# Kernel optimization log

Measured on AMD Instinct MI355X. Metric: run time of the kernel, lower is better.

The kernel has to match this reference:

```python
import jax, jax.numpy as jnp
import numpy as np

S, D, H, HD = 3072, 1280, 16, 80
FF = 4 * D
EPS = 1e-6


def layernorm(x, scale, bias):
    mu = jnp.mean(x, axis=-1, keepdims=True)
    var = jnp.mean(jnp.square(x - mu), axis=-1, keepdims=True)
    return (x - mu) * jax.lax.rsqrt(var + EPS) * scale + bias


def rotate_half(x):
    x1 = x[..., : x.shape[-1] // 2]
    x2 = x[..., x.shape[-1] // 2 :]
    return jnp.concatenate([-x2, x1], axis=-1)


def apply_rope(x, freqs):
    # x: (S,H,hd), freqs: (S,hd/2)
    cos = jnp.repeat(jnp.cos(freqs), 2, axis=-1)[:, None, :]  # (S,1,hd)
    sin = jnp.repeat(jnp.sin(freqs), 2, axis=-1)[:, None, :]
    return x * cos + rotate_half(x) * sin


def quick_gelu(x):
    return x * jax.nn.sigmoid(1.702 * x)


def setup_inputs() -> dict:
    key = jax.random.key(0)
    ks = jax.random.split(key, 12)
    s = 0.02
    return {
        "hidden_states": jax.random.normal(ks[0], (S, D), jnp.float32),
        "rotary_pos_emb": jax.random.normal(ks[1], (S, HD // 2), jnp.float32),
        "ln1_scale": jnp.ones((D,), jnp.float32),
        "ln1_bias": jnp.zeros((D,), jnp.float32),
        "ln2_scale": jnp.ones((D,), jnp.float32),
        "ln2_bias": jnp.zeros((D,), jnp.float32),
        "qkv_w": jax.random.normal(ks[2], (D, 3 * D), jnp.float32) * s,
        "qkv_b": jnp.zeros((3 * D,), jnp.float32),
        "proj_w": jax.random.normal(ks[3], (D, D), jnp.float32) * s,
        "proj_b": jnp.zeros((D,), jnp.float32),
        "fc1_w": jax.random.normal(ks[4], (D, FF), jnp.float32) * s,
        "fc1_b": jnp.zeros((FF,), jnp.float32),
        "fc2_w": jax.random.normal(ks[5], (FF, D), jnp.float32) * s,
        "fc2_b": jnp.zeros((D,), jnp.float32),
        "cu_seqlens": jnp.array([0, 1024, 2048, 3072], jnp.int32),
    }


def reference(hidden_states, rotary_pos_emb, ln1_scale, ln1_bias, ln2_scale,
              ln2_bias, qkv_w, qkv_b, proj_w, proj_b, fc1_w, fc1_b, fc2_w,
              fc2_b, cu_seqlens):
    x = hidden_states  # (S, D)
    h = layernorm(x, ln1_scale, ln1_bias)
    qkv = (h @ qkv_w + qkv_b).reshape(S, 3, H, HD)
    q, k, v = qkv[:, 0], qkv[:, 1], qkv[:, 2]  # each (S, H, hd)
    q = apply_rope(q, rotary_pos_emb)
    k = apply_rope(k, rotary_pos_emb)

    # block-diagonal varlen mask from cu_seqlens (same segment attends)
    ids = jnp.arange(S)
    seg = jnp.searchsorted(cu_seqlens, ids, side="right")  # (S,)
    valid = seg[:, None] == seg[None, :]  # (S, S)
    bias = jnp.where(valid, 0.0, jnp.finfo(q.dtype).min)

    scale = 1.0 / jnp.sqrt(jnp.asarray(HD, q.dtype))
    scores = jnp.einsum("qhd,khd->hqk", q, k) * scale + bias
    probs = jax.nn.softmax(scores.astype(jnp.float32), axis=-1).astype(q.dtype)
    attn = jnp.einsum("hqk,khd->qhd", probs, v).reshape(S, D)
    attn = attn @ proj_w + proj_b

    x = x + attn
    h2 = layernorm(x, ln2_scale, ln2_bias)
    mlp = quick_gelu(h2 @ fc1_w + fc1_b) @ fc2_w + fc2_b
    return x + mlp
```

## Files before the change

### kernel.cpp

```cpp
#include <hip/hip_runtime.h>

typedef __bf16 bf16x8 __attribute__((ext_vector_type(8)));
typedef float f32x4 __attribute__((ext_vector_type(4)));
typedef unsigned short u16;
typedef u16 u16x4 __attribute__((ext_vector_type(4)));
typedef u16 u16x8 __attribute__((ext_vector_type(8)));
typedef float float4v __attribute__((ext_vector_type(4)));

__device__ __forceinline__ u16 f2bf(float f) {
    __bf16 b = (__bf16)f;
    return __builtin_bit_cast(unsigned short, b);
}
__device__ __forceinline__ float bf2f(u16 x) {
    __bf16 b = __builtin_bit_cast(__bf16, x);
    return (float)b;
}

__device__ __forceinline__ void gld16(const void* g, void* l) {
    __builtin_amdgcn_global_load_lds((const __attribute__((address_space(1))) void*)g,
                                     (__attribute__((address_space(3))) void*)l, 16, 0, 0);
}

__device__ __forceinline__ int xcd_swz(int orig, int nwg) {
    const int q = nwg >> 3, r = nwg & 7;
    const int xcd = orig & 7, pos = orig >> 3;
    return (xcd < r ? xcd * (q + 1) : r * (q + 1) + (xcd - r) * q) + pos;
}

__global__ __launch_bounds__(256) void transpose_all_kernel(
    const float* __restrict__ qkvw, const float* __restrict__ projw,
    const float* __restrict__ fc1w, const float* __restrict__ fc2w,
    u16* __restrict__ qkvwT, u16* __restrict__ projwT,
    u16* __restrict__ fc1wT, u16* __restrict__ fc2wT)
{
    __shared__ u16 tile[64][65];
    int bid = blockIdx.x;
    const float* W; u16* WT; int K, N, nx;
    if (bid < 1200)      { W = qkvw;  WT = qkvwT;  K = 1280; N = 3840; nx = 60; }
    else if (bid < 1600) { bid -= 1200; W = projw; WT = projwT; K = 1280; N = 1280; nx = 20; }
    else if (bid < 3200) { bid -= 1600; W = fc1w;  WT = fc1wT;  K = 1280; N = 5120; nx = 80; }
    else                 { bid -= 3200; W = fc2w;  WT = fc2wT;  K = 5120; N = 1280; nx = 20; }
    const int tx = threadIdx.x & 63, ty = threadIdx.x >> 6;
    const int n0 = (bid % nx) * 64, k0 = (bid / nx) * 64;
    #pragma unroll
    for (int i = ty; i < 64; i += 4)
        tile[i][tx] = f2bf(W[(size_t)(k0 + i) * N + n0 + tx]);
    __syncthreads();
    #pragma unroll
    for (int i = ty; i < 64; i += 4)
        WT[(size_t)(n0 + i) * K + k0 + tx] = tile[tx][i];
}

__global__ __launch_bounds__(256) void ln_kernel(
    const float* __restrict__ x, const float* __restrict__ sc,
    const float* __restrict__ bias, u16* __restrict__ out)
{
    const int row = blockIdx.x, t = threadIdx.x;
    const float* xr = x + (size_t)row * 1280;
    float v[5], s1 = 0.f, s2 = 0.f;
    #pragma unroll
    for (int i = 0; i < 5; i++) {
        v[i] = xr[t + i * 256];
        s1 += v[i];
        s2 += v[i] * v[i];
    }
    #pragma unroll
    for (int off = 32; off; off >>= 1) {
        s1 += __shfl_down(s1, off);
        s2 += __shfl_down(s2, off);
    }
    __shared__ float rA[4], rB[4];
    if ((t & 63) == 0) { rA[t >> 6] = s1; rB[t >> 6] = s2; }
    __syncthreads();
    s1 = rA[0] + rA[1] + rA[2] + rA[3];
    s2 = rB[0] + rB[1] + rB[2] + rB[3];
    const float mu = s1 * (1.f / 1280.f);
    const float var = s2 * (1.f / 1280.f) - mu * mu;
    const float rstd = rsqrtf(var + 1e-6f);
    #pragma unroll
    for (int i = 0; i < 5; i++) {
        const int d = t + i * 256;
        out[(size_t)row * 1280 + d] = f2bf((v[i] - mu) * rstd * sc[d] + bias[d]);
    }
}

__global__ __launch_bounds__(256) void reduce4_ln_kernel(
    const float* __restrict__ parts, const float* __restrict__ bias,
    const float* __restrict__ res, const float* __restrict__ lns,
    const float* __restrict__ lnb, float* __restrict__ xmid,
    u16* __restrict__ h2, size_t MN)
{
    const int row = blockIdx.x, t = threadIdx.x;
    float v[5], s1 = 0.f, s2 = 0.f;
    #pragma unroll
    for (int i = 0; i < 5; i++) {
        const int d = t + i * 256;
        const size_t idx = (size_t)row * 1280 + d;
        float a = parts[idx] + parts[MN + idx] + parts[2 * MN + idx] + parts[3 * MN + idx]
                + res[idx] + bias[d];
        v[i] = a;
        xmid[idx] = a;
        s1 += a;
        s2 += a * a;
    }
    #pragma unroll
    for (int off = 32; off; off >>= 1) {
        s1 += __shfl_down(s1, off);
        s2 += __shfl_down(s2, off);
    }
    __shared__ float rA[4], rB[4];
    if ((t & 63) == 0) { rA[t >> 6] = s1; rB[t >> 6] = s2; }
    __syncthreads();
    s1 = rA[0] + rA[1] + rA[2] + rA[3];
    s2 = rB[0] + rB[1] + rB[2] + rB[3];
    const float mu = s1 * (1.f / 1280.f);
    const float var = s2 * (1.f / 1280.f) - mu * mu;
    const float rstd = rsqrtf(var + 1e-6f);
    #pragma unroll
    for (int i = 0; i < 5; i++) {
        const int d = t + i * 256;
        h2[(size_t)row * 1280 + d] = f2bf((v[i] - mu) * rstd * lns[d] + lnb[d]);
    }
}

template <int GELU, int OUTB, int SPLIT>
__global__ __launch_bounds__(512, 2) void gemm256_kernel(
    const u16* __restrict__ A, const u16* __restrict__ BT,
    const float* __restrict__ bias,
    float* __restrict__ outF, u16* __restrict__ outB,
    int M, int N, int K)
{
    __shared__ u16 As[2][256 * 64];
    __shared__ u16 Bs[2][256 * 64];
    const int tid = threadIdx.x, lane = tid & 63, wave = tid >> 6;
    const int nwg = gridDim.x * gridDim.y;
    const int bid = xcd_swz(blockIdx.y * gridDim.x + blockIdx.x, nwg);
    const int m0 = (bid / gridDim.x) * 256, n0 = (bid % gridDim.x) * 256;
    const int wr = wave >> 2, wc = wave & 3;
    const int wm = wr * 128, wn = wc * 64;
    const int lr = lane & 15, lh = lane >> 4;

    const int kchunk = K / SPLIT;
    const int kz = (SPLIT > 1) ? blockIdx.z : 0;
    const int kbeg = kz * kchunk;
    const int niter = kchunk >> 7;

    const int sr = lane >> 3;
    const int sc8 = (lane & 7) ^ sr;

    f32x4 acc[8][4] = {};
    bf16x8 bq[4][2];

    auto stgA = [&](int t, int h) {
        const int buf = t & 1;
        #pragma unroll
        for (int j = 0; j < 2; j++) {
            const int row = h * 128 + j * 64 + wave * 8 + sr;
            gld16(A + (size_t)(m0 + row) * K + kbeg + t * 64 + sc8 * 8,
                  &As[buf][h * 8192 + j * 4096 + wave * 512]);
        }
    };
    auto stgB = [&](int t, int h) {
        const int buf = t & 1;
        #pragma unroll
        for (int j = 0; j < 2; j++) {
            const int row = h * 128 + j * 64 + wave * 8 + sr;
            gld16(BT + (size_t)(n0 + row) * K + kbeg + t * 64 + sc8 * 8,
                  &Bs[buf][h * 8192 + j * 4096 + wave * 512]);
        }
    };

#define PHASE(BUF, Q, STGSTMT, WAITSTMT)                                        \
    {                                                                           \
        if ((Q) == 0) {                                                         \
            _Pragma("unroll") for (int ni = 0; ni < 4; ni++) {                  \
                const int row = wn + ni * 16 + lr;                              \
                _Pragma("unroll") for (int kk = 0; kk < 2; kk++)                \
                    bq[ni][kk] = *reinterpret_cast<const bf16x8*>(              \
                        &Bs[BUF][row * 64 + ((kk * 4 + lh) ^ (row & 7)) * 8]);  \
            }                                                                   \
        }                                                                       \
        bf16x8 afq[2][2];                                                       \
        _Pragma("unroll") for (int m2 = 0; m2 < 2; m2++) {                      \
            const int row = wm + (Q) * 32 + m2 * 16 + lr;                       \
            _Pragma("unroll") for (int kk = 0; kk < 2; kk++)                    \
                afq[m2][kk] = *reinterpret_cast<const bf16x8*>(                 \
                    &As[BUF][row * 64 + ((kk * 4 + lh) ^ (row & 7)) * 8]);      \
        }                                                                       \
        STGSTMT;                                                                \
        __builtin_amdgcn_s_barrier();                                           \
        asm volatile("s_waitcnt lgkmcnt(0)" ::: "memory");                      \
        __builtin_amdgcn_s_setprio(1);                                          \
        _Pragma("unroll") for (int kk = 0; kk < 2; kk++)                        \
            _Pragma("unroll") for (int m2 = 0; m2 < 2; m2++)                    \
                _Pragma("unroll") for (int ni = 0; ni < 4; ni++)                \
                    acc[(Q) * 2 + m2][ni] =                                     \
                        __builtin_amdgcn_mfma_f32_16x16x32_bf16(                \
                            afq[m2][kk], bq[ni][kk], acc[(Q) * 2 + m2][ni],     \
                            0, 0, 0);                                           \
        __builtin_amdgcn_s_setprio(0);                                          \
        WAITSTMT;                                                               \
        __builtin_amdgcn_s_barrier();                                           \
    }

    stgB(0, 0); stgB(0, 1);
    stgA(0, 0); stgA(0, 1);
    stgB(1, 0); stgB(1, 1);
    asm volatile("s_waitcnt vmcnt(4)" ::: "memory");
    __builtin_amdgcn_s_barrier();

    for (int i = 0; i < niter - 1; i++) {
        const int t0 = 2 * i, t1 = 2 * i + 1;
        PHASE(0, 0, stgA(t1, 0), (void)0);
        PHASE(0, 1, stgA(t1, 1), (void)0);
        PHASE(0, 2, stgB(t0 + 2, 0), (void)0);
        PHASE(0, 3, stgB(t0 + 2, 1),
              asm volatile("s_waitcnt vmcnt(4)" ::: "memory"));
        PHASE(1, 0, stgA(t0 + 2, 0), (void)0);
        PHASE(1, 1, stgA(t0 + 2, 1), (void)0);
        PHASE(1, 2, stgB(t1 + 2, 0), (void)0);
        PHASE(1, 3, stgB(t1 + 2, 1),
              asm volatile("s_waitcnt vmcnt(4)" ::: "memory"));
    }
    {
        const int t1 = 2 * niter - 1;
        PHASE(0, 0, stgA(t1, 0), (void)0);
        PHASE(0, 1, stgA(t1, 1), (void)0);
        PHASE(0, 2, (void)0, (void)0);
        PHASE(0, 3, (void)0,
              asm volatile("s_waitcnt vmcnt(0)" ::: "memory"));
        PHASE(1, 0, (void)0, (void)0);
        PHASE(1, 1, (void)0, (void)0);
        PHASE(1, 2, (void)0, (void)0);
        PHASE(1, 3, (void)0, (void)0);
    }
#undef PHASE

    if (SPLIT > 1) {
        float* pf = outF + (size_t)kz * M * N;
        #pragma unroll
        for (int mi = 0; mi < 8; mi++)
            #pragma unroll
            for (int ni = 0; ni < 4; ni++) {
                const int col = n0 + wn + ni * 16 + lr;
                #pragma unroll
                for (int r = 0; r < 4; r++) {
                    const int rowg = m0 + wm + mi * 16 + lh * 4 + r;
                    pf[(size_t)rowg * N + col] = acc[mi][ni][r];
                }
            }
        return;
    }

    #pragma unroll
    for (int mi = 0; mi < 8; mi++) {
        #pragma unroll
        for (int ni = 0; ni < 4; ni++) {
            const int col = n0 + wn + ni * 16 + lr;
            const float bv = bias[col];
            #pragma unroll
            for (int r = 0; r < 4; r++) {
                const int rowg = m0 + wm + mi * 16 + lh * 4 + r;
                float v = acc[mi][ni][r] + bv;
                if (GELU) v = v * (1.0f / (1.0f + __expf(-1.702f * v)));
                if (OUTB) outB[(size_t)rowg * N + col] = f2bf(v);
            }
        }
    }
}

template <int GELU, int RES, int OUTF, int OUTB, int SPLIT>
__global__ __launch_bounds__(256) void gemm_kernel(
    const u16* __restrict__ A, const u16* __restrict__ BT,
    const float* __restrict__ bias, const float* __restrict__ res,
    float* __restrict__ outF, u16* __restrict__ outB,
    int M, int N, int K)
{
    __shared__ u16 As[128 * 64];
    __shared__ u16 Bs[128 * 64];
    const int tid = threadIdx.x, lane = tid & 63, wave = tid >> 6;
    const int nwg = gridDim.x * gridDim.y;
    const int bid = xcd_swz(blockIdx.y * gridDim.x + blockIdx.x, nwg);
    const int m0 = (bid / gridDim.x) * 128, n0 = (bid % gridDim.x) * 128;
    const int wm = (wave >> 1) * 64, wn = (wave & 1) * 64;
    const int lr = lane & 15, lh = lane >> 4;
    const int srow = lane >> 3;
    const int schunk = (lane & 7) ^ (srow & 7);

    const int kchunk = K / SPLIT;
    const int kz = (SPLIT > 1) ? blockIdx.z : 0;
    const int kbeg = kz * kchunk, kend = kbeg + kchunk;

    f32x4 acc[4][4] = {};

    for (int k0 = kbeg; k0 < kend; k0 += 64) {
        #pragma unroll
        for (int s = 0; s < 4; s++) {
            const int seg = wave + s * 4;
            const int row = seg * 8 + srow;
            gld16(A + (size_t)(m0 + row) * K + k0 + schunk * 8, &As[seg * 512]);
            gld16(BT + (size_t)(n0 + row) * K + k0 + schunk * 8, &Bs[seg * 512]);
        }
        asm volatile("s_waitcnt vmcnt(0)" ::: "memory");
        __syncthreads();

        bf16x8 af[4][2], bfr[4][2];
        #pragma unroll
        for (int mi = 0; mi < 4; mi++) {
            const int row = wm + mi * 16 + lr;
            #pragma unroll
            for (int kk = 0; kk < 2; kk++) {
                const int cb = (kk * 64 + lh * 16) ^ ((row & 7) << 4);
                af[mi][kk] = *reinterpret_cast<const bf16x8*>((const char*)As + row * 128 + cb);
            }
        }
        #pragma unroll
        for (int ni = 0; ni < 4; ni++) {
            const int row = wn + ni * 16 + lr;
            #pragma unroll
            for (int kk = 0; kk < 2; kk++) {
                const int cb = (kk * 64 + lh * 16) ^ ((row & 7) << 4);
                bfr[ni][kk] = *reinterpret_cast<const bf16x8*>((const char*)Bs + row * 128 + cb);
            }
        }
        #pragma unroll
        for (int kk = 0; kk < 2; kk++)
            #pragma unroll
            for (int mi = 0; mi < 4; mi++)
                #pragma unroll
                for (int ni = 0; ni < 4; ni++)
                    acc[mi][ni] = __builtin_amdgcn_mfma_f32_16x16x32_bf16(
                        af[mi][kk], bfr[ni][kk], acc[mi][ni], 0, 0, 0);
        __syncthreads();
    }

    if (SPLIT > 1) {
        float* pf = outF + (size_t)kz * M * N;
        #pragma unroll
        for (int mi = 0; mi < 4; mi++)
            #pragma unroll
            for (int ni = 0; ni < 4; ni++) {
                const int col = n0 + wn + ni * 16 + lr;
                #pragma unroll
                for (int r = 0; r < 4; r++) {
                    const int rowg = m0 + wm + mi * 16 + lh * 4 + r;
                    pf[(size_t)rowg * N + col] = acc[mi][ni][r];
                }
            }
        return;
    }

    #pragma unroll
    for (int mi = 0; mi < 4; mi++) {
        #pragma unroll
        for (int ni = 0; ni < 4; ni++) {
            const int col = n0 + wn + ni * 16 + lr;
            const float bv = bias[col];
            #pragma unroll
            for (int r = 0; r < 4; r++) {
                const int rowg = m0 + wm + mi * 16 + lh * 4 + r;
                float v = acc[mi][ni][r] + bv;
                if (RES) v += res[(size_t)rowg * N + col];
                if (GELU) v = v * (1.0f / (1.0f + __expf(-1.702f * v)));
                if (OUTF) outF[(size_t)rowg * N + col] = v;
                if (OUTB) outB[(size_t)rowg * N + col] = f2bf(v);
            }
        }
    }
}

__global__ __launch_bounds__(256) void reduce4_kernel(
    const float* __restrict__ parts, const float* __restrict__ bias,
    const float* __restrict__ res, float* __restrict__ out, int N, size_t MN)
{
    const size_t i4 = ((size_t)blockIdx.x * 256 + threadIdx.x) * 4;
    if (i4 >= MN) return;
    float4v a = *reinterpret_cast<const float4v*>(parts + i4);
    a += *reinterpret_cast<const float4v*>(parts + MN + i4);
    a += *reinterpret_cast<const float4v*>(parts + 2 * MN + i4);
    a += *reinterpret_cast<const float4v*>(parts + 3 * MN + i4);
    a += *reinterpret_cast<const float4v*>(res + i4);
    const int col = (int)(i4 % N);
    a += *reinterpret_cast<const float4v*>(bias + col);
    *reinterpret_cast<float4v*>(out + i4) = a;
}

__global__ __launch_bounds__(256) void rope_kernel(
    const u16* __restrict__ qkv, const float* __restrict__ freqs,
    u16* __restrict__ qp, u16* __restrict__ kp, u16* __restrict__ vt)
{
    const int s = blockIdx.x, t = threadIdx.x;
    const float scale = 0.1118033988749895f;
    __shared__ float cs[40], sn[40];
    if (t < 40) {
        const float f = freqs[(size_t)s * 40 + t];
        cs[t] = cosf(f);
        sn[t] = sinf(f);
    }
    __syncthreads();
    const u16* row = qkv + (size_t)s * 3840;
    for (int i = t; i < 1280; i += 256) {
        const int h = i / 80, d = i % 80;
        const float c = cs[d >> 1], sv = sn[d >> 1];
        const float q0 = bf2f(row[i]);
        const float q1 = (d < 40) ? -bf2f(row[i + 40]) : bf2f(row[i - 40]);
        qp[((size_t)h * 3072 + s) * 96 + d] = f2bf((q0 * c + q1 * sv) * scale);
        const float k0 = bf2f(row[1280 + i]);
        const float k1 = (d < 40) ? -bf2f(row[1280 + i + 40]) : bf2f(row[1280 + i - 40]);
        kp[((size_t)h * 3072 + s) * 128 + d] = f2bf(k0 * c + k1 * sv);
        vt[((size_t)h * 80 + d) * 3072 + s] = row[2560 + i];
    }
    {
        const int h = t / 16, d = 80 + (t % 16);
        qp[((size_t)h * 3072 + s) * 96 + d] = 0;
    }
    for (int i = t; i < 768; i += 256) {
        const int h = i / 48, d = 80 + (i % 48);
        kp[((size_t)h * 3072 + s) * 128 + d] = 0;
    }
}

__global__ __launch_bounds__(256) void attn_kernel(
    const u16* __restrict__ qp, const u16* __restrict__ kp,
    const u16* __restrict__ vt, u16* __restrict__ attn_out)
{
    const int tid = threadIdx.x, lane = tid & 63, wave = tid >> 6;
    const int w = xcd_swz(blockIdx.x, 768);
    const int qt = w & 15;
    const int h = (w >> 4) & 15;
    const int sq = w >> 8;
    const int lr = lane & 15, lh = lane >> 4;
    const int qrow = sq * 1024 + qt * 64 + wave * 16;

    __shared__ u16 Ks[2][64 * 128];
    __shared__ u16 Vs[2][80 * 64];

    bf16x8 aq[3];
    {
        const u16* qb = qp + ((size_t)h * 3072 + qrow + lr) * 96 + lh * 8;
        #pragma unroll
        for (int d0 = 0; d0 < 3; d0++)
            aq[d0] = *reinterpret_cast<const bf16x8*>(qb + d0 * 32);
    }

    float m = -1e30f, l = 0.f;
    f32x4 acc[5] = {};

    const u16* kseg = kp + ((size_t)h * 3072 + sq * 1024) * 128;
    const u16* vseg = vt + (size_t)h * 80 * 3072 + sq * 1024;

    const int krow_l = lane >> 4;
    const int kch    = lane & 15;
    const int vrow_l = lane >> 3;
    const int vch    = lane & 7;

    auto stageK = [&](int t, int buf) {
        #pragma unroll
        for (int s = 0; s < 4; s++) {
            const int seg = wave + s * 4;
            const int row = seg * 4 + krow_l;
            gld16(kseg + (size_t)(t * 64 + row) * 128 + ((kch ^ (row & 7)) * 8),
                  &Ks[buf][seg * 512]);
        }
    };
    auto stageV = [&](int t, int buf) {
        #pragma unroll
        for (int s = 0; s < 3; s++) {
            const int seg = wave + s * 4;
            if (seg < 10) {
                const int row = seg * 8 + vrow_l;
                gld16(vseg + (size_t)row * 3072 + t * 64 + ((vch ^ (row & 7)) * 8),
                      &Vs[buf][seg * 512]);
            }
        }
    };

    stageK(0, 0);
    stageV(0, 0);
    asm volatile("s_waitcnt vmcnt(0)" ::: "memory");
    __syncthreads();

    const int prow = wave * 16 + lr;
    const int psw = prow & 7;

    for (int t = 0; t < 16; t++) {
        const int cur = t & 1;
        if (t < 15) {
            stageK(t + 1, cur ^ 1);
            stageV(t + 1, cur ^ 1);
        }

        f32x4 sc[4] = {};
        #pragma unroll
        for (int c = 0; c < 4; c++) {
            #pragma unroll
            for (int d0 = 0; d0 < 3; d0++) {
                const int row = c * 16 + lr;
                const int rb = row * 256 + (((d0 * 4 + lh) ^ (row & 7)) << 4);
                bf16x8 kf = *reinterpret_cast<const bf16x8*>((const char*)Ks[cur] + rb);
                sc[c] = __builtin_amdgcn_mfma_f32_16x16x32_bf16(kf, aq[d0], sc[c], 0, 0, 0);
            }
        }

        float pmax = sc[0][0];
        #pragma unroll
        for (int c = 0; c < 4; c++)
            #pragma unroll
            for (int r = 0; r < 4; r++)
                pmax = fmaxf(pmax, sc[c][r]);
        pmax = fmaxf(pmax, __shfl_xor(pmax, 16));
        pmax = fmaxf(pmax, __shfl_xor(pmax, 32));

        if (!__all(pmax - m <= 8.0f)) {
            const float mn = fmaxf(m, pmax);
            const float fac = __expf(m - mn);
            m = mn;
            l *= fac;
            #pragma unroll
            for (int df = 0; df < 5; df++)
                #pragma unroll
                for (int r = 0; r < 4; r++)
                    acc[df][r] *= fac;
        }

        float p[4][4], rs = 0.f;
        #pragma unroll
        for (int c = 0; c < 4; c++)
            #pragma unroll
            for (int r = 0; r < 4; r++) {
                p[c][r] = __expf(sc[c][r] - m);
                rs += p[c][r];
            }
        rs += __shfl_xor(rs, 16);
        rs += __shfl_xor(rs, 32);
        l += rs;

        char* pb = (char*)Ks[cur] + prow * 256;
        const int prd = ((12 + lh) ^ psw) << 4;

        #pragma unroll
        for (int cc = 0; cc < 2; cc++) {
            u16x4 pw;
            #pragma unroll
            for (int r = 0; r < 4; r++)
                pw[r] = f2bf(p[cc][r]);
            *reinterpret_cast<u16x4*>(
                pb + (((12 + cc * 2 + (lh >> 1)) ^ psw) << 4) + (lh & 1) * 8) = pw;
        }
        asm volatile("s_waitcnt lgkmcnt(0)" ::: "memory");
        {
            bf16x8 pa = *reinterpret_cast<const bf16x8*>(pb + prd);
            asm volatile("s_waitcnt lgkmcnt(0)" ::: "memory");
            #pragma unroll
            for (int df = 0; df < 5; df++) {
                const int row = df * 16 + lr;
                const int vb = row * 128 + ((lh ^ (row & 7)) << 4);
                bf16x8 vf = *reinterpret_cast<const bf16x8*>((const char*)Vs[cur] + vb);
                acc[df] = __builtin_amdgcn_mfma_f32_16x16x32_bf16(vf, pa, acc[df], 0, 0, 0);
            }
        }
        #pragma unroll
        for (int cc = 0; cc < 2; cc++) {
            u16x4 pw;
            #pragma unroll
            for (int r = 0; r < 4; r++)
                pw[r] = f2bf(p[2 + cc][r]);
            *reinterpret_cast<u16x4*>(
                pb + (((12 + cc * 2 + (lh >> 1)) ^ psw) << 4) + (lh & 1) * 8) = pw;
        }
        asm volatile("s_waitcnt lgkmcnt(0)" ::: "memory");
        {
            bf16x8 pa = *reinterpret_cast<const bf16x8*>(pb + prd);
            #pragma unroll
            for (int df = 0; df < 5; df++) {
                const int row = df * 16 + lr;
                const int vb = row * 128 + (((4 + lh) ^ (row & 7)) << 4);
                bf16x8 vf = *reinterpret_cast<const bf16x8*>((const char*)Vs[cur] + vb);
                acc[df] = __builtin_amdgcn_mfma_f32_16x16x32_bf16(vf, pa, acc[df], 0, 0, 0);
            }
        }

        asm volatile("s_waitcnt vmcnt(0)" ::: "memory");
        __syncthreads();
    }

    const float invl = 1.0f / l;
    u16* orow = attn_out + (size_t)(qrow + lr) * 1280 + h * 80;
    #pragma unroll
    for (int df = 0; df < 5; df++) {
        u16x4 o;
        #pragma unroll
        for (int r = 0; r < 4; r++)
            o[r] = f2bf(acc[df][r] * invl);
        *reinterpret_cast<u16x4*>(orow + df * 16 + lh * 4) = o;
    }
}

extern "C" void kernel_launch(void* const* d_in, const int* in_sizes, int n_in,
                              void* d_out, int out_size, void* d_ws, size_t ws_size,
                              hipStream_t stream) {
    const float* hidden = (const float*)d_in[0];
    const float* rot    = (const float*)d_in[1];
    const float* ln1s   = (const float*)d_in[2];
    const float* ln1b   = (const float*)d_in[3];
    const float* ln2s   = (const float*)d_in[4];
    const float* ln2b   = (const float*)d_in[5];
    const float* qkvw   = (const float*)d_in[6];
    const float* qkvb   = (const float*)d_in[7];
    const float* projw  = (const float*)d_in[8];
    const float* projb  = (const float*)d_in[9];
    const float* fc1w   = (const float*)d_in[10];
    const float* fc1b   = (const float*)d_in[11];
    const float* fc2w   = (const float*)d_in[12];
    const float* fc2b   = (const float*)d_in[13];
    float* out = (float*)d_out;

    char* p = (char*)d_ws;
    auto alloc = [&](size_t n) { char* r = p; p += (n + 255) & ~(size_t)255; return r; };
    u16* qkvwT  = (u16*)alloc((size_t)3840 * 1280 * 2);
    u16* projwT = (u16*)alloc((size_t)1280 * 1280 * 2);
    u16* fc1wT  = (u16*)alloc((size_t)5120 * 1280 * 2);
    u16* fc2wT  = (u16*)alloc((size_t)1280 * 5120 * 2);
    u16* hbuf   = (u16*)alloc((size_t)3072 * 1280 * 2);
    u16* qkvbf  = (u16*)alloc((size_t)3072 * 5120 * 2);
    u16* attnb  = (u16*)alloc((size_t)3072 * 1280 * 2);
    float* xmid = (float*)alloc((size_t)3072 * 1280 * 4);
    float* parts = (float*)alloc((size_t)4 * 3072 * 1280 * 4);
    u16* qp2 = (u16*)parts;
    u16* kp2 = qp2 + (size_t)16 * 3072 * 96;
    u16* vt2 = kp2 + (size_t)16 * 3072 * 128;
    u16* h2   = hbuf;
    u16* mlp1 = qkvbf;
    const size_t MN = (size_t)3072 * 1280;

    transpose_all_kernel<<<4800, 256, 0, stream>>>(
        qkvw, projw, fc1w, fc2w, qkvwT, projwT, fc1wT, fc2wT);

    ln_kernel<<<3072, 256, 0, stream>>>(hidden, ln1s, ln1b, hbuf);
    gemm256_kernel<0, 1, 1><<<dim3(15, 12), 512, 0, stream>>>(
        hbuf, qkvwT, qkvb, nullptr, qkvbf, 3072, 3840, 1280);
    rope_kernel<<<3072, 256, 0, stream>>>(qkvbf, rot, qp2, kp2, vt2);
    attn_kernel<<<768, 256, 0, stream>>>(qp2, kp2, vt2, attnb);
    gemm_kernel<0, 0, 1, 0, 4><<<dim3(10, 24, 4), 256, 0, stream>>>(
        attnb, projwT, projb, nullptr, parts, nullptr, 3072, 1280, 1280);
    reduce4_ln_kernel<<<3072, 256, 0, stream>>>(
        parts, projb, hidden, ln2s, ln2b, xmid, h2, MN);
    gemm256_kernel<1, 1, 1><<<dim3(20, 12), 512, 0, stream>>>(
        h2, fc1wT, fc1b, nullptr, mlp1, 3072, 5120, 1280);
    gemm256_kernel<0, 0, 4><<<dim3(5, 12, 4), 512, 0, stream>>>(
        mlp1, fc2wT, fc2b, parts, nullptr, 3072, 1280, 5120);
    reduce4_kernel<<<(int)(MN / 4 / 256), 256, 0, stream>>>(parts, fc2b, xmid, out, 1280, MN);
}
```

Baseline: 289.5 us.

## Store split-K partials in bf16 and precompute LDS/global address pointers

Split-K partial sums from the projection and fc2 GEMMs are now written and read as bf16 instead of fp32. This halves the traffic for the partials buffer and for the reduce kernels that sum them. Separately, the GEMM and attention kernels precompute per-thread global and LDS address pointers outside their loops, which cuts the integer address arithmetic inside the inner loops. Rounding the partials to bf16 adds accuracy loss to the residual path.

```diff
diff --git a/kernel.cpp b/kernel.cpp
--- a/kernel.cpp
+++ b/kernel.cpp
@@ -85,7 +85,7 @@
 }
 
 __global__ __launch_bounds__(256) void reduce4_ln_kernel(
-    const float* __restrict__ parts, const float* __restrict__ bias,
+    const u16* __restrict__ parts, const float* __restrict__ bias,
     const float* __restrict__ res, const float* __restrict__ lns,
     const float* __restrict__ lnb, float* __restrict__ xmid,
     u16* __restrict__ h2, size_t MN)
@@ -96,7 +96,8 @@
     for (int i = 0; i < 5; i++) {
         const int d = t + i * 256;
         const size_t idx = (size_t)row * 1280 + d;
-        float a = parts[idx] + parts[MN + idx] + parts[2 * MN + idx] + parts[3 * MN + idx]
+        float a = bf2f(parts[idx]) + bf2f(parts[MN + idx])
+                + bf2f(parts[2 * MN + idx]) + bf2f(parts[3 * MN + idx])
                 + res[idx] + bias[d];
         v[i] = a;
         xmid[idx] = a;
@@ -121,6 +122,24 @@
         const int d = t + i * 256;
         h2[(size_t)row * 1280 + d] = f2bf((v[i] - mu) * rstd * lns[d] + lnb[d]);
     }
+}
+
+__global__ __launch_bounds__(256) void reduce4b_kernel(
+    const u16* __restrict__ parts, const float* __restrict__ bias,
+    const float* __restrict__ res, float* __restrict__ out, int N, size_t MN)
+{
+    const size_t i4 = ((size_t)blockIdx.x * 256 + threadIdx.x) * 4;
+    if (i4 >= MN) return;
+    float4v a = *reinterpret_cast<const float4v*>(res + i4);
+    #pragma unroll
+    for (int p = 0; p < 4; p++) {
+        u16x4 v = *reinterpret_cast<const u16x4*>(parts + p * MN + i4);
+        #pragma unroll
+        for (int r = 0; r < 4; r++) a[r] += bf2f(v[r]);
+    }
+    const int col = (int)(i4 % N);
+    a += *reinterpret_cast<const float4v*>(bias + col);
+    *reinterpret_cast<float4v*>(out + i4) = a;
 }
 
 template <int GELU, int OUTB, int SPLIT>
@@ -139,6 +158,7 @@
     const int wr = wave >> 2, wc = wave & 3;
     const int wm = wr * 128, wn = wc * 64;
     const int lr = lane & 15, lh = lane >> 4;
+    const int xa = lr & 7;
 
     const int kchunk = K / SPLIT;
     const int kz = (SPLIT > 1) ? blockIdx.z : 0;
@@ -151,42 +171,47 @@
     f32x4 acc[8][4] = {};
     bf16x8 bq[4][2];
 
-    auto stgA = [&](int t, int h) {
-        const int buf = t & 1;
+    const char* aRd[2] = {
+        (const char*)As + (wm + lr) * 128 + ((0 + lh) ^ xa) * 16,
+        (const char*)As + (wm + lr) * 128 + ((4 + lh) ^ xa) * 16 };
+    const char* bRd[2] = {
+        (const char*)Bs + (wn + lr) * 128 + ((0 + lh) ^ xa) * 16,
+        (const char*)Bs + (wn + lr) * 128 + ((4 + lh) ^ xa) * 16 };
+
+    const u16 *aG[2][2], *bG[2][2];
+    #pragma unroll
+    for (int h = 0; h < 2; h++)
         #pragma unroll
         for (int j = 0; j < 2; j++) {
             const int row = h * 128 + j * 64 + wave * 8 + sr;
-            gld16(A + (size_t)(m0 + row) * K + kbeg + t * 64 + sc8 * 8,
-                  &As[buf][h * 8192 + j * 4096 + wave * 512]);
-        }
+            aG[h][j] = A + (size_t)(m0 + row) * K + kbeg + sc8 * 8;
+            bG[h][j] = BT + (size_t)(n0 + row) * K + kbeg + sc8 * 8;
+        }
+
+    auto stgA = [&](int t, int h) {
+        u16* d = (u16*)As + (t & 1) * 16384 + h * 8192 + wave * 512;
+        gld16(aG[h][0] + (size_t)t * 64, d);
+        gld16(aG[h][1] + (size_t)t * 64, d + 4096);
     };
     auto stgB = [&](int t, int h) {
-        const int buf = t & 1;
-        #pragma unroll
-        for (int j = 0; j < 2; j++) {
-            const int row = h * 128 + j * 64 + wave * 8 + sr;
-            gld16(BT + (size_t)(n0 + row) * K + kbeg + t * 64 + sc8 * 8,
-                  &Bs[buf][h * 8192 + j * 4096 + wave * 512]);
-        }
+        u16* d = (u16*)Bs + (t & 1) * 16384 + h * 8192 + wave * 512;
+        gld16(bG[h][0] + (size_t)t * 64, d);
+        gld16(bG[h][1] + (size_t)t * 64, d + 4096);
     };
 
 #define PHASE(BUF, Q, STGSTMT, WAITSTMT)                                        \
     {                                                                           \
         if ((Q) == 0) {                                                         \
-            _Pragma("unroll") for (int ni = 0; ni < 4; ni++) {                  \
-                const int row = wn + ni * 16 + lr;                              \
+            _Pragma("unroll") for (int ni = 0; ni < 4; ni++)                    \
                 _Pragma("unroll") for (int kk = 0; kk < 2; kk++)                \
                     bq[ni][kk] = *reinterpret_cast<const bf16x8*>(              \
-                        &Bs[BUF][row * 64 + ((kk * 4 + lh) ^ (row & 7)) * 8]);  \
-            }                                                                   \
+                        bRd[kk] + (BUF) * 32768 + ni * 2048);                   \
         }                                                                       \
         bf16x8 afq[2][2];                                                       \
-        _Pragma("unroll") for (int m2 = 0; m2 < 2; m2++) {                      \
-            const int row = wm + (Q) * 32 + m2 * 16 + lr;                       \
+        _Pragma("unroll") for (int m2 = 0; m2 < 2; m2++)                        \
             _Pragma("unroll") for (int kk = 0; kk < 2; kk++)                    \
                 afq[m2][kk] = *reinterpret_cast<const bf16x8*>(                 \
-                    &As[BUF][row * 64 + ((kk * 4 + lh) ^ (row & 7)) * 8]);      \
-        }                                                                       \
+                    aRd[kk] + (BUF) * 32768 + (Q) * 4096 + m2 * 2048);          \
         STGSTMT;                                                                \
         __builtin_amdgcn_s_barrier();                                           \
         asm volatile("s_waitcnt lgkmcnt(0)" ::: "memory");                      \
@@ -237,7 +262,7 @@
 #undef PHASE
 
     if (SPLIT > 1) {
-        float* pf = outF + (size_t)kz * M * N;
+        u16* pf = outB + (size_t)kz * M * N;
         #pragma unroll
         for (int mi = 0; mi < 8; mi++)
             #pragma unroll
@@ -246,7 +271,7 @@
                 #pragma unroll
                 for (int r = 0; r < 4; r++) {
                     const int rowg = m0 + wm + mi * 16 + lh * 4 + r;
-                    pf[(size_t)rowg * N + col] = acc[mi][ni][r];
+                    pf[(size_t)rowg * N + col] = f2bf(acc[mi][ni][r]);
                 }
             }
         return;
@@ -269,12 +294,10 @@
     }
 }
 
-template <int GELU, int RES, int OUTF, int OUTB, int SPLIT>
+template <int SPLIT>
 __global__ __launch_bounds__(256) void gemm_kernel(
     const u16* __restrict__ A, const u16* __restrict__ BT,
-    const float* __restrict__ bias, const float* __restrict__ res,
-    float* __restrict__ outF, u16* __restrict__ outB,
-    int M, int N, int K)
+    u16* __restrict__ partB, int M, int N, int K)
 {
     __shared__ u16 As[128 * 64];
     __shared__ u16 Bs[128 * 64];
@@ -284,45 +307,54 @@
     const int m0 = (bid / gridDim.x) * 128, n0 = (bid % gridDim.x) * 128;
     const int wm = (wave >> 1) * 64, wn = (wave & 1) * 64;
     const int lr = lane & 15, lh = lane >> 4;
+    const int xa = lr & 7;
     const int srow = lane >> 3;
     const int schunk = (lane & 7) ^ (srow & 7);
 
     const int kchunk = K / SPLIT;
     const int kz = (SPLIT > 1) ? blockIdx.z : 0;
-    const int kbeg = kz * kchunk, kend = kbeg + kchunk;
+    const int kbeg = kz * kchunk;
+
+    const u16 *aG[4], *bG[4];
+    u16 *dA[4], *dB[4];
+    #pragma unroll
+    for (int s = 0; s < 4; s++) {
+        const int seg = wave + s * 4;
+        const int row = seg * 8 + srow;
+        aG[s] = A + (size_t)(m0 + row) * K + kbeg + schunk * 8;
+        bG[s] = BT + (size_t)(n0 + row) * K + kbeg + schunk * 8;
+        dA[s] = As + seg * 512;
+        dB[s] = Bs + seg * 512;
+    }
+    const char* aRd[2] = {
+        (const char*)As + (wm + lr) * 128 + ((0 + lh) ^ xa) * 16,
+        (const char*)As + (wm + lr) * 128 + ((4 + lh) ^ xa) * 16 };
+    const char* bRd[2] = {
+        (const char*)Bs + (wn + lr) * 128 + ((0 + lh) ^ xa) * 16,
+        (const char*)Bs + (wn + lr) * 128 + ((4 + lh) ^ xa) * 16 };
 
     f32x4 acc[4][4] = {};
 
-    for (int k0 = kbeg; k0 < kend; k0 += 64) {
+    for (int ko = 0; ko < kchunk; ko += 64) {
         #pragma unroll
         for (int s = 0; s < 4; s++) {
-            const int seg = wave + s * 4;
-            const int row = seg * 8 + srow;
-            gld16(A + (size_t)(m0 + row) * K + k0 + schunk * 8, &As[seg * 512]);
-            gld16(BT + (size_t)(n0 + row) * K + k0 + schunk * 8, &Bs[seg * 512]);
+            gld16(aG[s] + ko, dA[s]);
+            gld16(bG[s] + ko, dB[s]);
         }
         asm volatile("s_waitcnt vmcnt(0)" ::: "memory");
         __syncthreads();
 
         bf16x8 af[4][2], bfr[4][2];
         #pragma unroll
-        for (int mi = 0; mi < 4; mi++) {
-            const int row = wm + mi * 16 + lr;
-            #pragma unroll
-            for (int kk = 0; kk < 2; kk++) {
-                const int cb = (kk * 64 + lh * 16) ^ ((row & 7) << 4);
-                af[mi][kk] = *reinterpret_cast<const bf16x8*>((const char*)As + row * 128 + cb);
-            }
-        }
-        #pragma unroll
-        for (int ni = 0; ni < 4; ni++) {
-            const int row = wn + ni * 16 + lr;
-            #pragma unroll
-            for (int kk = 0; kk < 2; kk++) {
-                const int cb = (kk * 64 + lh * 16) ^ ((row & 7) << 4);
-                bfr[ni][kk] = *reinterpret_cast<const bf16x8*>((const char*)Bs + row * 128 + cb);
-            }
-        }
+        for (int mi = 0; mi < 4; mi++)
+            #pragma unroll
+            for (int kk = 0; kk < 2; kk++)
+                af[mi][kk] = *reinterpret_cast<const bf16x8*>(aRd[kk] + mi * 2048);
+        #pragma unroll
+        for (int ni = 0; ni < 4; ni++)
+            #pragma unroll
+            for (int kk = 0; kk < 2; kk++)
+                bfr[ni][kk] = *reinterpret_cast<const bf16x8*>(bRd[kk] + ni * 2048);
         #pragma unroll
         for (int kk = 0; kk < 2; kk++)
             #pragma unroll
@@ -334,55 +366,18 @@
         __syncthreads();
     }
 
-    if (SPLIT > 1) {
-        float* pf = outF + (size_t)kz * M * N;
-        #pragma unroll
-        for (int mi = 0; mi < 4; mi++)
-            #pragma unroll
-            for (int ni = 0; ni < 4; ni++) {
-                const int col = n0 + wn + ni * 16 + lr;
-                #pragma unroll
-                for (int r = 0; r < 4; r++) {
-                    const int rowg = m0 + wm + mi * 16 + lh * 4 + r;
-                    pf[(size_t)rowg * N + col] = acc[mi][ni][r];
-                }
-            }
-        return;
-    }
-
-    #pragma unroll
-    for (int mi = 0; mi < 4; mi++) {
+    u16* pf = partB + (size_t)kz * M * N;
+    #pragma unroll
+    for (int mi = 0; mi < 4; mi++)
         #pragma unroll
         for (int ni = 0; ni < 4; ni++) {
             const int col = n0 + wn + ni * 16 + lr;
-            const float bv = bias[col];
             #pragma unroll
             for (int r = 0; r < 4; r++) {
                 const int rowg = m0 + wm + mi * 16 + lh * 4 + r;
-                float v = acc[mi][ni][r] + bv;
-                if (RES) v += res[(size_t)rowg * N + col];
-                if (GELU) v = v * (1.0f / (1.0f + __expf(-1.702f * v)));
-                if (OUTF) outF[(size_t)rowg * N + col] = v;
-                if (OUTB) outB[(size_t)rowg * N + col] = f2bf(v);
+                pf[(size_t)rowg * N + col] = f2bf(acc[mi][ni][r]);
             }
         }
-    }
-}
-
-__global__ __launch_bounds__(256) void reduce4_kernel(
-    const float* __restrict__ parts, const float* __restrict__ bias,
-    const float* __restrict__ res, float* __restrict__ out, int N, size_t MN)
-{
-    const size_t i4 = ((size_t)blockIdx.x * 256 + threadIdx.x) * 4;
-    if (i4 >= MN) return;
-    float4v a = *reinterpret_cast<const float4v*>(parts + i4);
-    a += *reinterpret_cast<const float4v*>(parts + MN + i4);
-    a += *reinterpret_cast<const float4v*>(parts + 2 * MN + i4);
-    a += *reinterpret_cast<const float4v*>(parts + 3 * MN + i4);
-    a += *reinterpret_cast<const float4v*>(res + i4);
-    const int col = (int)(i4 % N);
-    a += *reinterpret_cast<const float4v*>(bias + col);
-    *reinterpret_cast<float4v*>(out + i4) = a;
 }
 
 __global__ __launch_bounds__(256) void rope_kernel(
@@ -430,6 +425,7 @@
     const int h = (w >> 4) & 15;
     const int sq = w >> 8;
     const int lr = lane & 15, lh = lane >> 4;
+    const int xa = lr & 7;
     const int qrow = sq * 1024 + qt * 64 + wave * 16;
 
     __shared__ u16 Ks[2][64 * 128];
@@ -454,25 +450,33 @@
     const int vrow_l = lane >> 3;
     const int vch    = lane & 7;
 
+    const u16 *kG[4], *vG[3];
+    u16 *kD[4], *vD[3];
+    #pragma unroll
+    for (int s = 0; s < 4; s++) {
+        const int seg = wave + s * 4;
+        const int row = seg * 4 + krow_l;
+        kG[s] = kseg + (size_t)row * 128 + ((kch ^ (row & 7)) * 8);
+        kD[s] = (u16*)Ks + seg * 512;
+    }
+    #pragma unroll
+    for (int s = 0; s < 3; s++) {
+        const int seg = wave + s * 4;
+        const int row = (seg < 10) ? seg * 8 + vrow_l : 0;
+        vG[s] = vseg + (size_t)row * 3072 + ((vch ^ (row & 7)) * 8);
+        vD[s] = (u16*)Vs + seg * 512;
+    }
+
     auto stageK = [&](int t, int buf) {
         #pragma unroll
-        for (int s = 0; s < 4; s++) {
-            const int seg = wave + s * 4;
-            const int row = seg * 4 + krow_l;
-            gld16(kseg + (size_t)(t * 64 + row) * 128 + ((kch ^ (row & 7)) * 8),
-                  &Ks[buf][seg * 512]);
-        }
+        for (int s = 0; s < 4; s++)
+            gld16(kG[s] + (size_t)t * 8192, kD[s] + buf * 8192);
     };
     auto stageV = [&](int t, int buf) {
         #pragma unroll
-        for (int s = 0; s < 3; s++) {
-            const int seg = wave + s * 4;
-            if (seg < 10) {
-                const int row = seg * 8 + vrow_l;
-                gld16(vseg + (size_t)row * 3072 + t * 64 + ((vch ^ (row & 7)) * 8),
-                      &Vs[buf][seg * 512]);
-            }
-        }
+        for (int s = 0; s < 3; s++)
+            if (wave + s * 4 < 10)
+                gld16(vG[s] + t * 64, vD[s] + buf * 5120);
     };
 
     stageK(0, 0);
@@ -480,11 +484,22 @@
     asm volatile("s_waitcnt vmcnt(0)" ::: "memory");
     __syncthreads();
 
+    const char* kRd[3] = {
+        (const char*)Ks + lr * 256 + ((0 + lh) ^ xa) * 16,
+        (const char*)Ks + lr * 256 + ((4 + lh) ^ xa) * 16,
+        (const char*)Ks + lr * 256 + ((8 + lh) ^ xa) * 16 };
+    const char* vRd[2] = {
+        (const char*)Vs + lr * 128 + ((0 + lh) ^ xa) * 16,
+        (const char*)Vs + lr * 128 + ((4 + lh) ^ xa) * 16 };
+
     const int prow = wave * 16 + lr;
     const int psw = prow & 7;
+    const char* pBase = (const char*)Ks + prow * 256;
+    const int prd = ((12 + lh) ^ psw) << 4;
 
     for (int t = 0; t < 16; t++) {
         const int cur = t & 1;
+        const int curK = cur * 16384, curV = cur * 10240;
         if (t < 15) {
             stageK(t + 1, cur ^ 1);
             stageV(t + 1, cur ^ 1);
@@ -495,9 +510,7 @@
         for (int c = 0; c < 4; c++) {
             #pragma unroll
             for (int d0 = 0; d0 < 3; d0++) {
-                const int row = c * 16 + lr;
-                const int rb = row * 256 + (((d0 * 4 + lh) ^ (row & 7)) << 4);
-                bf16x8 kf = *reinterpret_cast<const bf16x8*>((const char*)Ks[cur] + rb);
+                bf16x8 kf = *reinterpret_cast<const bf16x8*>(kRd[d0] + curK + c * 4096);
                 sc[c] = __builtin_amdgcn_mfma_f32_16x16x32_bf16(kf, aq[d0], sc[c], 0, 0, 0);
             }
         }
@@ -535,8 +548,7 @@
         rs += __shfl_xor(rs, 32);
         l += rs;
 
-        char* pb = (char*)Ks[cur] + prow * 256;
-        const int prd = ((12 + lh) ^ psw) << 4;
+        char* pb = (char*)pBase + curK;
 
         #pragma unroll
         for (int cc = 0; cc < 2; cc++) {
@@ -553,9 +565,7 @@
             asm volatile("s_waitcnt lgkmcnt(0)" ::: "memory");
             #pragma unroll
             for (int df = 0; df < 5; df++) {
-                const int row = df * 16 + lr;
-                const int vb = row * 128 + ((lh ^ (row & 7)) << 4);
-                bf16x8 vf = *reinterpret_cast<const bf16x8*>((const char*)Vs[cur] + vb);
+                bf16x8 vf = *reinterpret_cast<const bf16x8*>(vRd[0] + curV + df * 2048);
                 acc[df] = __builtin_amdgcn_mfma_f32_16x16x32_bf16(vf, pa, acc[df], 0, 0, 0);
             }
         }
@@ -573,9 +583,7 @@
             bf16x8 pa = *reinterpret_cast<const bf16x8*>(pb + prd);
             #pragma unroll
             for (int df = 0; df < 5; df++) {
-                const int row = df * 16 + lr;
-                const int vb = row * 128 + (((4 + lh) ^ (row & 7)) << 4);
-                bf16x8 vf = *reinterpret_cast<const bf16x8*>((const char*)Vs[cur] + vb);
+                bf16x8 vf = *reinterpret_cast<const bf16x8*>(vRd[1] + curV + df * 2048);
                 acc[df] = __builtin_amdgcn_mfma_f32_16x16x32_bf16(vf, pa, acc[df], 0, 0, 0);
             }
         }
@@ -625,8 +633,8 @@
     u16* qkvbf  = (u16*)alloc((size_t)3072 * 5120 * 2);
     u16* attnb  = (u16*)alloc((size_t)3072 * 1280 * 2);
     float* xmid = (float*)alloc((size_t)3072 * 1280 * 4);
-    float* parts = (float*)alloc((size_t)4 * 3072 * 1280 * 4);
-    u16* qp2 = (u16*)parts;
+    u16* partsB = (u16*)alloc((size_t)4 * 3072 * 1280 * 2);
+    u16* qp2 = partsB;
     u16* kp2 = qp2 + (size_t)16 * 3072 * 96;
     u16* vt2 = kp2 + (size_t)16 * 3072 * 128;
     u16* h2   = hbuf;
@@ -641,13 +649,13 @@
         hbuf, qkvwT, qkvb, nullptr, qkvbf, 3072, 3840, 1280);
     rope_kernel<<<3072, 256, 0, stream>>>(qkvbf, rot, qp2, kp2, vt2);
     attn_kernel<<<768, 256, 0, stream>>>(qp2, kp2, vt2, attnb);
-    gemm_kernel<0, 0, 1, 0, 4><<<dim3(10, 24, 4), 256, 0, stream>>>(
-        attnb, projwT, projb, nullptr, parts, nullptr, 3072, 1280, 1280);
+    gemm_kernel<4><<<dim3(10, 24, 4), 256, 0, stream>>>(
+        attnb, projwT, partsB, 3072, 1280, 1280);
     reduce4_ln_kernel<<<3072, 256, 0, stream>>>(
-        parts, projb, hidden, ln2s, ln2b, xmid, h2, MN);
+        partsB, projb, hidden, ln2s, ln2b, xmid, h2, MN);
     gemm256_kernel<1, 1, 1><<<dim3(20, 12), 512, 0, stream>>>(
         h2, fc1wT, fc1b, nullptr, mlp1, 3072, 5120, 1280);
     gemm256_kernel<0, 0, 4><<<dim3(5, 12, 4), 512, 0, stream>>>(
-        mlp1, fc2wT, fc2b, parts, nullptr, 3072, 1280, 5120);
-    reduce4_kernel<<<(int)(MN / 4 / 256), 256, 0, stream>>>(parts, fc2b, xmid, out, 1280, MN);
-}
+        mlp1, fc2wT, fc2b, nullptr, partsB, 3072, 1280, 5120);
+    reduce4b_kernel<<<(int)(MN / 4 / 256), 256, 0, stream>>>(partsB, fc2b, xmid, out, 1280, MN);
+}
```

New measurement: 277.5 us. 1.04x faster.
